# Kernel tuning notes

Hardware: AMD Instinct MI355X
Metric: run time of the kernel (lower is better)

The kernel has to match this reference:

```python
import jax, jax.numpy as jnp
import numpy as np

NQ = 4          # n_qubits
NL = 2          # ansatz layers in timestep circuit
T = 200         # n_timesteps
DEG = 3         # qsvt_degree
B = 2048        # batch
NROTS = 5 * NQ * NL     # 40
QFF_NROTS = 5 * NQ      # 20
DIM = 2 ** NQ

# --- batched 2x2 gate matrices (h = theta/2, shape (N,)) ---
def _rx(h):
    c = jnp.cos(h).astype(jnp.complex64)
    s = (-1j * jnp.sin(h)).astype(jnp.complex64)
    return jnp.stack([jnp.stack([c, s], -1), jnp.stack([s, c], -1)], -2)

def _ry(h):
    c, s = jnp.cos(h), jnp.sin(h)
    return jnp.stack([jnp.stack([c, -s], -1), jnp.stack([s, c], -1)], -2).astype(jnp.complex64)

def _rz(h):
    e = jnp.exp(-1j * h.astype(jnp.complex64))
    z = jnp.zeros_like(e)
    return jnp.stack([jnp.stack([e, z], -1), jnp.stack([z, jnp.conj(e)], -1)], -2)

# state layout: (N, 2, 2, ..., 2) with axis 1+w = qubit w (PennyLane wire ordering)
def _apply_1q(state, mat, w):
    st = jnp.moveaxis(state, 1 + w, -1)
    st = jnp.einsum('bij,b...j->b...i', mat, st)
    return jnp.moveaxis(st, -1, 1 + w)

def _apply_crx(state, h, cw, tw):
    m = _rx(h)
    st = jnp.moveaxis(state, (1 + cw, 1 + tw), (-2, -1))  # (..., control, target)
    s1 = jnp.einsum('bij,b...j->b...i', m, st[..., 1, :])  # RX on target iff control=1
    st = jnp.stack([st[..., 0, :], s1], axis=-2)
    return jnp.moveaxis(st, (-2, -1), (1 + cw, 1 + tw))

def _ansatz(state, params, layers):
    # params: (N, 5*NQ*layers) float
    half = params * 0.5
    idx = 0
    for _ in range(layers):
        for i in range(NQ):
            state = _apply_1q(state, _rx(half[:, idx]), i)
            state = _apply_1q(state, _ry(half[:, idx + 1]), i)
            state = _apply_1q(state, _rz(half[:, idx + 2]), i)
            idx += 3
        for i in range(NQ):
            state = _apply_crx(state, half[:, idx], i, (i + 1) % NQ)
            idx += 1
        for i in range(NQ - 1, -1, -1):
            state = _apply_crx(state, half[:, idx], i, (i - 1) % NQ)
            idx += 1
    return state

def _lcu(base, tparams, coeffs):
    # base: (B, DIM) complex; tparams: (B, T, NROTS); coeffs: (B, T) complex
    b, t, r = tparams.shape
    flat = tparams.reshape(b * t, r)
    st = jnp.repeat(base, t, axis=0).reshape((b * t,) + (2,) * NQ)
    st = _ansatz(st, flat, NL)
    ev = st.reshape(b, t, DIM)
    return jnp.einsum('bti,bt->bi', ev, coeffs)

def _expvals(state):
    # returns (B, 3*NQ): [<X_0..X_{n-1}>, <Y...>, <Z...>]
    outs_x, outs_y, outs_z = [], [], []
    red = tuple(range(1, NQ))  # reduce all non-batch, non-target axes after moveaxis
    for i in range(NQ):
        st = jnp.moveaxis(state, 1 + i, -1)
        s0, s1 = st[..., 0], st[..., 1]
        z = jnp.conj(s0) * s1
        outs_x.append(jnp.sum(2.0 * jnp.real(z), axis=red))
        outs_y.append(jnp.sum(2.0 * jnp.imag(z), axis=red))
        outs_z.append(jnp.sum(jnp.abs(s0) ** 2 - jnp.abs(s1) ** 2, axis=red))
    return jnp.stack(outs_x + outs_y + outs_z, axis=1).astype(jnp.float32)

def _forward(timestep_params, poly_coeffs, mix_re, mix_im, qff_params):
    b = timestep_params.shape[0]
    base = jnp.zeros((b, DIM), jnp.complex64).at[:, 0].set(1.0)
    coeffs = jnp.broadcast_to((mix_re + 1j * mix_im).astype(jnp.complex64), (b, T))
    # QSVT polynomial: acc = sum_k c_k (LCU)^k |0>
    acc = poly_coeffs[0] * base
    work = base
    for k in range(1, DEG + 1):
        work = _lcu(work, timestep_params, coeffs)
        acc = acc + poly_coeffs[k] * work
    acc = acc / jnp.sum(jnp.abs(poly_coeffs))  # L1 norm of poly coeffs
    norm = jnp.linalg.norm(acc, axis=1, keepdims=True)
    st = (acc / (norm + 1e-9)).reshape((b,) + (2,) * NQ)
    qp = jnp.broadcast_to(qff_params, (b, QFF_NROTS))
    st = _ansatz(st, qp, 1)
    return _expvals(st)

def setup_inputs() -> dict:
    key = jax.random.key(0)
    k1, k2, k3, k4, k5 = jax.random.split(key, 5)
    return {
        'timestep_params': jax.random.uniform(k1, (B, T, NROTS), jnp.float32),
        'poly_coeffs': jax.random.uniform(k2, (DEG + 1,), jnp.float32),
        'mix_re': jax.random.uniform(k3, (T,), jnp.float32),
        'mix_im': jax.random.uniform(k4, (T,), jnp.float32),
        'qff_params': jax.random.uniform(k5, (QFF_NROTS,), jnp.float32),
    }

def reference(timestep_params, poly_coeffs, mix_re, mix_im, qff_params):
    return _forward(timestep_params, poly_coeffs, mix_re, mix_im, qff_params)
```

## Files before the change

### kernel.cpp

```cpp
#include <hip/hip_runtime.h>
#include <math.h>

#define TSTEPS 200
#define NROTS  40
#define BLK    128
#define DEG    3

typedef float v2 __attribute__((ext_vector_type(2)));

__device__ __forceinline__ v2 mk2(float a, float b) { v2 r; r.x = a; r.y = b; return r; }

#if __has_builtin(__builtin_elementwise_fma)
#define FMA2(a, b, c) __builtin_elementwise_fma((a), (b), (c))
#else
__device__ __forceinline__ v2 FMA2(v2 a, v2 b, v2 c) {
#pragma clang fp contract(fast)
    return a * b + c;
}
#endif

__device__ __forceinline__ v2 sin2(v2 h) { return mk2(__sinf(h.x), __sinf(h.y)); }
__device__ __forceinline__ v2 cos2(v2 h) { return mk2(__cosf(h.x), __cosf(h.y)); }

__device__ __forceinline__ void fsc(float h, float& s, float& c) {
    s = __sinf(h); c = __cosf(h);
}

__device__ __forceinline__ void make_u2(v2 h1, v2 h2, v2 h3, v2* u) {
    v2 s1 = sin2(h1), c1 = cos2(h1);
    v2 s2 = sin2(h2), c2 = cos2(h2);
    v2 s3 = sin2(h3), c3 = cos2(h3);
    v2 A = c1 * c2, Bv = s1 * s2, C = c1 * s2, D = s1 * c2;
    u[0] = FMA2(s3, Bv, c3 * A);
    u[1] = FMA2(-s3, A, c3 * Bv);
    u[2] = -FMA2(s3, D, c3 * C);
    u[3] = FMA2(-c3, D, s3 * C);
}

__device__ __forceinline__ void fsc2(v2 h, v2* sc) { sc[0] = sin2(h); sc[1] = cos2(h); }

template<int BIT>
__device__ __forceinline__ void g_u2(v2* V, const v2* u) {
    const v2 u00r = u[0], u00i = u[1], u01r = u[2], u01i = u[3];
    #pragma unroll
    for (int p = 0; p < 16; ++p) {
        if (p & BIT) continue;
        const int q = p | BIT;
        v2 a0r = V[p], a0i = V[16 + p], a1r = V[q], a1i = V[16 + q];
        v2 t0 = u00r * a0r;
        t0 = FMA2(-u00i, a0i, t0);
        t0 = FMA2( u01r, a1r, t0);
        t0 = FMA2(-u01i, a1i, t0);
        v2 t1 = u00r * a0i;
        t1 = FMA2( u00i, a0r, t1);
        t1 = FMA2( u01r, a1i, t1);
        t1 = FMA2( u01i, a1r, t1);
        v2 t2 = u00r * a1r;
        t2 = FMA2( u00i, a1i, t2);
        t2 = FMA2(-u01r, a0r, t2);
        t2 = FMA2(-u01i, a0i, t2);
        v2 t3 = u00r * a1i;
        t3 = FMA2(-u00i, a1r, t3);
        t3 = FMA2(-u01r, a0i, t3);
        t3 = FMA2( u01i, a0r, t3);
        V[p] = t0; V[16 + p] = t1; V[q] = t2; V[16 + q] = t3;
    }
}

template<int CBIT, int TBIT>
__device__ __forceinline__ void g_crx_pre(v2* V, v2 s, v2 c) {
    #pragma unroll
    for (int p = 0; p < 16; ++p) {
        if (!(p & CBIT) || (p & TBIT)) continue;
        const int q = p | TBIT;
        v2 a0r = V[p], a0i = V[16 + p], a1r = V[q], a1i = V[16 + q];
        V[p]      = FMA2( s, a1i, c * a0r);
        V[16 + p] = FMA2(-s, a1r, c * a0i);
        V[q]      = FMA2( s, a0i, c * a1r);
        V[16 + q] = FMA2(-s, a0r, c * a1i);
    }
}

__device__ __forceinline__ void apply_layer_pre(v2* V, const v2 (&u)[4][4],
                                                const v2 (&cs)[8][2]) {
    g_u2<8>(V, u[0]); g_u2<4>(V, u[1]); g_u2<2>(V, u[2]); g_u2<1>(V, u[3]);
    g_crx_pre<8, 4>(V, cs[0][0], cs[0][1]);
    g_crx_pre<4, 2>(V, cs[1][0], cs[1][1]);
    g_crx_pre<2, 1>(V, cs[2][0], cs[2][1]);
    g_crx_pre<1, 8>(V, cs[3][0], cs[3][1]);
    g_crx_pre<1, 2>(V, cs[4][0], cs[4][1]);
    g_crx_pre<2, 4>(V, cs[5][0], cs[5][1]);
    g_crx_pre<4, 8>(V, cs[6][0], cs[6][1]);
    g_crx_pre<8, 1>(V, cs[7][0], cs[7][1]);
}

template<int S, int HALF>
__device__ __forceinline__ void rstep(float* V, int lane) {
    const bool hi = (lane >> S) & 1;
    #pragma unroll
    for (int j = 0; j < HALF; ++j) {
        float send = hi ? V[j] : V[j + HALF];
        float keep = hi ? V[j + HALF] : V[j];
        V[j] = keep + __shfl_xor(send, 1 << S, 64);
    }
}

extern "C" __global__ void __launch_bounds__(BLK, 1)
qac_kernel(const float* __restrict__ tp,
           const float* __restrict__ poly,
           const float* __restrict__ mixr,
           const float* __restrict__ mixi,
           const float* __restrict__ qff,
           float* __restrict__ out)
{
    __shared__ float s_red[2][32];
    __shared__ float s_w[32];
    __shared__ float s_acc[32];

    const int b    = blockIdx.x;
    const int tid  = threadIdx.x;
    const int lane = tid & 63;
    const int wv   = tid >> 6;

    if (tid < 32) {
        s_w[tid]   = (tid == 0) ? 1.f : 0.f;
        s_acc[tid] = (tid == 0) ? poly[0] : 0.f;
    }

    const bool vB = (tid + BLK) < TSTEPS;
    const int  tB = vB ? (tid + BLK) : (TSTEPS - 1);
    v2 cr_ = mk2(mixr[tid], vB ? mixr[tid + BLK] : 0.f);
    v2 ci_ = mk2(mixi[tid], vB ? mixi[tid + BLK] : 0.f);

    const float4* p4A = (const float4*)(tp + (size_t)b * (TSTEPS * NROTS) + tid * NROTS);
    const float4* p4B = (const float4*)(tp + (size_t)b * (TSTEPS * NROTS) + tB * NROTS);

    v2 tu[2][4][4];
    v2 tc[2][8][2];
    #pragma unroll
    for (int L = 0; L < 2; ++L) {
        float4 a0 = p4A[5*L+0], a1 = p4A[5*L+1], a2 = p4A[5*L+2], a3 = p4A[5*L+3], a4 = p4A[5*L+4];
        float4 b0 = p4B[5*L+0], b1 = p4B[5*L+1], b2 = p4B[5*L+2], b3 = p4B[5*L+3], b4 = p4B[5*L+4];
        make_u2(mk2(0.5f*a0.x, 0.5f*b0.x), mk2(0.5f*a0.y, 0.5f*b0.y), mk2(0.5f*a0.z, 0.5f*b0.z), tu[L][0]);
        make_u2(mk2(0.5f*a0.w, 0.5f*b0.w), mk2(0.5f*a1.x, 0.5f*b1.x), mk2(0.5f*a1.y, 0.5f*b1.y), tu[L][1]);
        make_u2(mk2(0.5f*a1.z, 0.5f*b1.z), mk2(0.5f*a1.w, 0.5f*b1.w), mk2(0.5f*a2.x, 0.5f*b2.x), tu[L][2]);
        make_u2(mk2(0.5f*a2.y, 0.5f*b2.y), mk2(0.5f*a2.z, 0.5f*b2.z), mk2(0.5f*a2.w, 0.5f*b2.w), tu[L][3]);
        fsc2(mk2(0.5f*a3.x, 0.5f*b3.x), tc[L][0]);
        fsc2(mk2(0.5f*a3.y, 0.5f*b3.y), tc[L][1]);
        fsc2(mk2(0.5f*a3.z, 0.5f*b3.z), tc[L][2]);
        fsc2(mk2(0.5f*a3.w, 0.5f*b3.w), tc[L][3]);
        fsc2(mk2(0.5f*a4.x, 0.5f*b4.x), tc[L][4]);
        fsc2(mk2(0.5f*a4.y, 0.5f*b4.y), tc[L][5]);
        fsc2(mk2(0.5f*a4.z, 0.5f*b4.z), tc[L][6]);
        fsc2(mk2(0.5f*a4.w, 0.5f*b4.w), tc[L][7]);
    }

    const int vidx = ((lane & 1) << 4) | ((lane & 2) << 2) | (lane & 4) |
                     ((lane & 8) >> 2) | ((lane & 16) >> 4);

    __syncthreads();

    #pragma unroll 1
    for (int k = 1; k <= DEG; ++k) {
        v2 V[32];
        #pragma unroll
        for (int i = 0; i < 32; ++i) { float t = s_w[i]; V[i] = mk2(t, t); }

        apply_layer_pre(V, tu[0], tc[0]);
        apply_layer_pre(V, tu[1], tc[1]);

        #pragma unroll
        for (int i = 0; i < 16; ++i) {
            v2 r = V[i], im = V[16 + i];
            V[i]      = FMA2(-im, ci_, r * cr_);
            V[16 + i] = FMA2( im, cr_, r * ci_);
        }

        float S[32];
        #pragma unroll
        for (int i = 0; i < 32; ++i) S[i] = V[i].x + V[i].y;

        rstep<0, 16>(S, lane);
        rstep<1, 8>(S, lane);
        rstep<2, 4>(S, lane);
        rstep<3, 2>(S, lane);
        rstep<4, 1>(S, lane);
        float tot = S[0] + __shfl_xor(S[0], 32, 64);
        if (lane < 32) s_red[wv][vidx] = tot;

        __syncthreads();
        if (tid < 32) {
            float r = s_red[0][tid] + s_red[1][tid];
            s_w[tid] = r;
            s_acc[tid] += poly[k] * r;
        }
        __syncthreads();
    }

    if (tid < 16) {
        const int l = tid;
        float l1 = fabsf(poly[0]) + fabsf(poly[1]) + fabsf(poly[2]) + fabsf(poly[3]);
        float inv = 1.f / l1;
        float ar = s_acc[l] * inv, ai = s_acc[16 + l] * inv;
        float n2 = ar * ar + ai * ai;
        #pragma unroll
        for (int o = 1; o < 16; o <<= 1) n2 += __shfl_xor(n2, o, 64);
        float sc = 1.f / (sqrtf(n2) + 1e-9f);
        ar *= sc; ai *= sc;

        float s, c, pr, pi, se, ce, t0;
        #pragma unroll
        for (int w = 0; w < 4; ++w) {
            const int BIT = 8 >> w;
            fsc(0.5f * qff[3 * w + 0], s, c);
            pr = __shfl_xor(ar, BIT, 64); pi = __shfl_xor(ai, BIT, 64);
            t0 = c * ar + s * pi; ai = c * ai - s * pr; ar = t0;
            fsc(0.5f * qff[3 * w + 1], s, c);
            pr = __shfl_xor(ar, BIT, 64); pi = __shfl_xor(ai, BIT, 64);
            se = (l & BIT) ? s : -s;
            t0 = c * ar + se * pr; ai = c * ai + se * pi; ar = t0;
            fsc(0.5f * qff[3 * w + 2], s, c);
            se = (l & BIT) ? s : -s;
            t0 = c * ar - se * ai; ai = c * ai + se * ar; ar = t0;
        }
        #define CRXF(CB, TB, hp) { fsc(0.5f * (hp), s, c);                        \
            pr = __shfl_xor(ar, TB, 64); pi = __shfl_xor(ai, TB, 64);             \
            ce = (l & CB) ? c : 1.f; se = (l & CB) ? s : 0.f;                     \
            t0 = ce * ar + se * pi; ai = ce * ai - se * pr; ar = t0; }
        CRXF(8, 4, qff[12]) CRXF(4, 2, qff[13]) CRXF(2, 1, qff[14]) CRXF(1, 8, qff[15])
        CRXF(1, 2, qff[16]) CRXF(2, 4, qff[17]) CRXF(4, 8, qff[18]) CRXF(8, 1, qff[19])
        #undef CRXF

        float* o = out + (size_t)b * 12;
        #pragma unroll
        for (int w = 0; w < 4; ++w) {
            const int BIT = 8 >> w;
            pr = __shfl_xor(ar, BIT, 64); pi = __shfl_xor(ai, BIT, 64);
            float m = (l & BIT) ? 0.f : 1.f;
            float X = m * 2.f * (ar * pr + ai * pi);
            float Y = m * 2.f * (ar * pi - ai * pr);
            float Z = m * (ar * ar + ai * ai - pr * pr - pi * pi);
            #pragma unroll
            for (int of = 1; of < 16; of <<= 1) {
                X += __shfl_xor(X, of, 64);
                Y += __shfl_xor(Y, of, 64);
                Z += __shfl_xor(Z, of, 64);
            }
            if (l == 0) { o[w] = X; o[4 + w] = Y; o[8 + w] = Z; }
        }
    }
}

extern "C" void kernel_launch(void* const* d_in, const int* in_sizes, int n_in,
                              void* d_out, int out_size, void* d_ws, size_t ws_size,
                              hipStream_t stream) {
    const float* tp   = (const float*)d_in[0];
    const float* poly = (const float*)d_in[1];
    const float* mixr = (const float*)d_in[2];
    const float* mixi = (const float*)d_in[3];
    const float* qff  = (const float*)d_in[4];
    float* out = (float*)d_out;
    const int B = in_sizes[0] / (TSTEPS * NROTS);
    qac_kernel<<<dim3(B), dim3(BLK), 0, stream>>>(tp, poly, mixr, mixi, qff, out);
}
```

Baseline: 145.6 us.

## Recompute gate matrices per QSVT pass to cut registers and raise occupancy

The kernel no longer precomputes all 2-layer gate matrices into registers once. Each of the three QSVT passes now reloads the timestep parameters from global memory and recomputes the sin/cos gate coefficients right before applying each gate, inside a noinline helper. Launch bounds go from 1 to 4 blocks per CU. The aim is lower register pressure so more waves can run concurrently, at the cost of three times the transcendental work and parameter loads, plus function-call overhead.

```diff
diff --git a/kernel.cpp b/kernel.cpp
--- a/kernel.cpp
+++ b/kernel.cpp
@@ -81,19 +81,6 @@
     }
 }
 
-__device__ __forceinline__ void apply_layer_pre(v2* V, const v2 (&u)[4][4],
-                                                const v2 (&cs)[8][2]) {
-    g_u2<8>(V, u[0]); g_u2<4>(V, u[1]); g_u2<2>(V, u[2]); g_u2<1>(V, u[3]);
-    g_crx_pre<8, 4>(V, cs[0][0], cs[0][1]);
-    g_crx_pre<4, 2>(V, cs[1][0], cs[1][1]);
-    g_crx_pre<2, 1>(V, cs[2][0], cs[2][1]);
-    g_crx_pre<1, 8>(V, cs[3][0], cs[3][1]);
-    g_crx_pre<1, 2>(V, cs[4][0], cs[4][1]);
-    g_crx_pre<2, 4>(V, cs[5][0], cs[5][1]);
-    g_crx_pre<4, 8>(V, cs[6][0], cs[6][1]);
-    g_crx_pre<8, 1>(V, cs[7][0], cs[7][1]);
-}
-
 template<int S, int HALF>
 __device__ __forceinline__ void rstep(float* V, int lane) {
     const bool hi = (lane >> S) & 1;
@@ -105,7 +92,71 @@
     }
 }
 
-extern "C" __global__ void __launch_bounds__(BLK, 1)
+__device__ __noinline__ void qsvt_pass(
+    const float4* __restrict__ p4A, const float4* __restrict__ p4B,
+    v2 cr_, v2 ci_, float pk, int tid, int lane, int wv, int vidx,
+    float* __restrict__ s_w, float (* __restrict__ s_red)[32],
+    float* __restrict__ s_acc)
+{
+    v2 V[32];
+    #pragma unroll
+    for (int i = 0; i < 32; ++i) { float t = s_w[i]; V[i] = mk2(t, t); }
+
+    #pragma unroll
+    for (int L = 0; L < 2; ++L) {
+        const float4 a0 = p4A[5*L+0], a1 = p4A[5*L+1], a2 = p4A[5*L+2];
+        const float4 b0 = p4B[5*L+0], b1 = p4B[5*L+1], b2 = p4B[5*L+2];
+        v2 u[4];
+        make_u2(mk2(0.5f*a0.x, 0.5f*b0.x), mk2(0.5f*a0.y, 0.5f*b0.y), mk2(0.5f*a0.z, 0.5f*b0.z), u);
+        g_u2<8>(V, u);
+        make_u2(mk2(0.5f*a0.w, 0.5f*b0.w), mk2(0.5f*a1.x, 0.5f*b1.x), mk2(0.5f*a1.y, 0.5f*b1.y), u);
+        g_u2<4>(V, u);
+        make_u2(mk2(0.5f*a1.z, 0.5f*b1.z), mk2(0.5f*a1.w, 0.5f*b1.w), mk2(0.5f*a2.x, 0.5f*b2.x), u);
+        g_u2<2>(V, u);
+        make_u2(mk2(0.5f*a2.y, 0.5f*b2.y), mk2(0.5f*a2.z, 0.5f*b2.z), mk2(0.5f*a2.w, 0.5f*b2.w), u);
+        g_u2<1>(V, u);
+        const float4 a3 = p4A[5*L+3], a4 = p4A[5*L+4];
+        const float4 b3 = p4B[5*L+3], b4 = p4B[5*L+4];
+        v2 sc[2];
+        fsc2(mk2(0.5f*a3.x, 0.5f*b3.x), sc); g_crx_pre<8, 4>(V, sc[0], sc[1]);
+        fsc2(mk2(0.5f*a3.y, 0.5f*b3.y), sc); g_crx_pre<4, 2>(V, sc[0], sc[1]);
+        fsc2(mk2(0.5f*a3.z, 0.5f*b3.z), sc); g_crx_pre<2, 1>(V, sc[0], sc[1]);
+        fsc2(mk2(0.5f*a3.w, 0.5f*b3.w), sc); g_crx_pre<1, 8>(V, sc[0], sc[1]);
+        fsc2(mk2(0.5f*a4.x, 0.5f*b4.x), sc); g_crx_pre<1, 2>(V, sc[0], sc[1]);
+        fsc2(mk2(0.5f*a4.y, 0.5f*b4.y), sc); g_crx_pre<2, 4>(V, sc[0], sc[1]);
+        fsc2(mk2(0.5f*a4.z, 0.5f*b4.z), sc); g_crx_pre<4, 8>(V, sc[0], sc[1]);
+        fsc2(mk2(0.5f*a4.w, 0.5f*b4.w), sc); g_crx_pre<8, 1>(V, sc[0], sc[1]);
+    }
+
+    #pragma unroll
+    for (int i = 0; i < 16; ++i) {
+        v2 r = V[i], im = V[16 + i];
+        V[i]      = FMA2(-im, ci_, r * cr_);
+        V[16 + i] = FMA2( im, cr_, r * ci_);
+    }
+
+    float S[32];
+    #pragma unroll
+    for (int i = 0; i < 32; ++i) S[i] = V[i].x + V[i].y;
+
+    rstep<0, 16>(S, lane);
+    rstep<1, 8>(S, lane);
+    rstep<2, 4>(S, lane);
+    rstep<3, 2>(S, lane);
+    rstep<4, 1>(S, lane);
+    float tot = S[0] + __shfl_xor(S[0], 32, 64);
+    if (lane < 32) s_red[wv][vidx] = tot;
+
+    __syncthreads();
+    if (tid < 32) {
+        float r = s_red[0][tid] + s_red[1][tid];
+        s_w[tid] = r;
+        s_acc[tid] += pk * r;
+    }
+    __syncthreads();
+}
+
+extern "C" __global__ void __launch_bounds__(BLK, 4)
 qac_kernel(const float* __restrict__ tp,
            const float* __restrict__ poly,
            const float* __restrict__ mixr,
@@ -135,26 +186,6 @@
     const float4* p4A = (const float4*)(tp + (size_t)b * (TSTEPS * NROTS) + tid * NROTS);
     const float4* p4B = (const float4*)(tp + (size_t)b * (TSTEPS * NROTS) + tB * NROTS);
 
-    v2 tu[2][4][4];
-    v2 tc[2][8][2];
-    #pragma unroll
-    for (int L = 0; L < 2; ++L) {
-        float4 a0 = p4A[5*L+0], a1 = p4A[5*L+1], a2 = p4A[5*L+2], a3 = p4A[5*L+3], a4 = p4A[5*L+4];
-        float4 b0 = p4B[5*L+0], b1 = p4B[5*L+1], b2 = p4B[5*L+2], b3 = p4B[5*L+3], b4 = p4B[5*L+4];
-        make_u2(mk2(0.5f*a0.x, 0.5f*b0.x), mk2(0.5f*a0.y, 0.5f*b0.y), mk2(0.5f*a0.z, 0.5f*b0.z), tu[L][0]);
-        make_u2(mk2(0.5f*a0.w, 0.5f*b0.w), mk2(0.5f*a1.x, 0.5f*b1.x), mk2(0.5f*a1.y, 0.5f*b1.y), tu[L][1]);
-        make_u2(mk2(0.5f*a1.z, 0.5f*b1.z), mk2(0.5f*a1.w, 0.5f*b1.w), mk2(0.5f*a2.x, 0.5f*b2.x), tu[L][2]);
-        make_u2(mk2(0.5f*a2.y, 0.5f*b2.y), mk2(0.5f*a2.z, 0.5f*b2.z), mk2(0.5f*a2.w, 0.5f*b2.w), tu[L][3]);
-        fsc2(mk2(0.5f*a3.x, 0.5f*b3.x), tc[L][0]);
-        fsc2(mk2(0.5f*a3.y, 0.5f*b3.y), tc[L][1]);
-        fsc2(mk2(0.5f*a3.z, 0.5f*b3.z), tc[L][2]);
-        fsc2(mk2(0.5f*a3.w, 0.5f*b3.w), tc[L][3]);
-        fsc2(mk2(0.5f*a4.x, 0.5f*b4.x), tc[L][4]);
-        fsc2(mk2(0.5f*a4.y, 0.5f*b4.y), tc[L][5]);
-        fsc2(mk2(0.5f*a4.z, 0.5f*b4.z), tc[L][6]);
-        fsc2(mk2(0.5f*a4.w, 0.5f*b4.w), tc[L][7]);
-    }
-
     const int vidx = ((lane & 1) << 4) | ((lane & 2) << 2) | (lane & 4) |
                      ((lane & 8) >> 2) | ((lane & 16) >> 4);
 
@@ -162,39 +193,8 @@
 
     #pragma unroll 1
     for (int k = 1; k <= DEG; ++k) {
-        v2 V[32];
-        #pragma unroll
-        for (int i = 0; i < 32; ++i) { float t = s_w[i]; V[i] = mk2(t, t); }
-
-        apply_layer_pre(V, tu[0], tc[0]);
-        apply_layer_pre(V, tu[1], tc[1]);
-
-        #pragma unroll
-        for (int i = 0; i < 16; ++i) {
-            v2 r = V[i], im = V[16 + i];
-            V[i]      = FMA2(-im, ci_, r * cr_);
-            V[16 + i] = FMA2( im, cr_, r * ci_);
-        }
-
-        float S[32];
-        #pragma unroll
-        for (int i = 0; i < 32; ++i) S[i] = V[i].x + V[i].y;
-
-        rstep<0, 16>(S, lane);
-        rstep<1, 8>(S, lane);
-        rstep<2, 4>(S, lane);
-        rstep<3, 2>(S, lane);
-        rstep<4, 1>(S, lane);
-        float tot = S[0] + __shfl_xor(S[0], 32, 64);
-        if (lane < 32) s_red[wv][vidx] = tot;
-
-        __syncthreads();
-        if (tid < 32) {
-            float r = s_red[0][tid] + s_red[1][tid];
-            s_w[tid] = r;
-            s_acc[tid] += poly[k] * r;
-        }
-        __syncthreads();
+        qsvt_pass(p4A, p4B, cr_, ci_, poly[k], tid, lane, wv, vidx,
+                  s_w, s_red, s_acc);
     }
 
     if (tid < 16) {
```

After: 223.2 us. 1.53x slower.
